# Optimization experiments

Hardware: AMD Instinct MI355X
Metric: run time of the kernel (lower is better)

The kernel has to match this reference:

```python
import jax, jax.numpy as jnp
import numpy as np

LIDAR_MAX_X = 32.0
LIDAR_MAX_Y = 32.0


def bilinear_grid_sample(value, grid):
    """torch.nn.functional.grid_sample, mode='bilinear', padding_mode='zeros',
    align_corners=False.
    value: (B, C, H, W); grid: (B, Q, P, 2) in [-1, 1] (x=width, y=height).
    Returns (B, C, Q, P)."""
    B, C, H, W = value.shape
    x = (grid[..., 0] + 1.0) * (W / 2) - 0.5  # (B,Q,P) unnormalized col
    y = (grid[..., 1] + 1.0) * (H / 2) - 0.5  # (B,Q,P) unnormalized row
    x0 = jnp.floor(x)
    y0 = jnp.floor(y)
    x1 = x0 + 1.0
    y1 = y0 + 1.0
    wx1 = x - x0
    wx0 = 1.0 - wx1
    wy1 = y - y0
    wy0 = 1.0 - wy1
    vflat = value.reshape(B, C, H * W)

    def gather(ix, iy):
        valid = (ix >= 0) & (ix <= W - 1) & (iy >= 0) & (iy <= H - 1)
        ixc = jnp.clip(ix, 0, W - 1).astype(jnp.int32)
        iyc = jnp.clip(iy, 0, H - 1).astype(jnp.int32)
        idx = iyc * W + ixc  # (B,Q,P)
        g = jax.vmap(lambda v, i: v[:, i])(vflat, idx)  # (B,C,Q,P)
        return g * valid[:, None, :, :].astype(value.dtype)

    out = (gather(x0, y0) * (wx0 * wy0)[:, None]
           + gather(x1, y0) * (wx1 * wy0)[:, None]
           + gather(x0, y1) * (wx0 * wy1)[:, None]
           + gather(x1, y1) * (wx1 * wy1)[:, None])
    return out


def setup_inputs() -> dict:
    key = jax.random.key(0)
    ks = jax.random.split(key, 10)
    bs, Q, P, D = 16, 1024, 8, 256
    Cin, H, W = 64, 128, 128
    queries = jax.random.normal(ks[0], (bs, Q, D), dtype=jnp.float32)
    # scale so trajectory points span the +/-32m BEV extent
    traj_points = jax.random.normal(ks[1], (bs, Q, P, 2), dtype=jnp.float32) * 20.0
    bev_feature = jax.random.normal(ks[2], (bs, Cin, H, W), dtype=jnp.float32)
    spatial_shape = jnp.array([H, W], dtype=jnp.int64)
    attn_w = jax.random.normal(ks[3], (P, D), dtype=jnp.float32) * 0.02
    attn_b = jnp.zeros((P,), dtype=jnp.float32)
    conv_w = jax.random.normal(ks[4], (256, Cin, 3, 3), dtype=jnp.float32) * 0.05
    conv_b = jnp.zeros((256,), dtype=jnp.float32)
    out_w = jax.random.normal(ks[5], (D, D), dtype=jnp.float32) * (1.0 / np.sqrt(D))
    out_b = jnp.zeros((D,), dtype=jnp.float32)
    return {"queries": queries, "traj_points": traj_points,
            "bev_feature": bev_feature, "spatial_shape": spatial_shape,
            "attn_w": attn_w, "attn_b": attn_b,
            "conv_w": conv_w, "conv_b": conv_b,
            "out_w": out_w, "out_b": out_b}


def reference(queries, traj_points, bev_feature, spatial_shape,
              attn_w, attn_b, conv_w, conv_b, out_w, out_b):
    # normalize trajectory to [-1,1] and swap (y,x) -> (x,y) grid order
    grid = jnp.stack([traj_points[..., 1] / LIDAR_MAX_X,
                      traj_points[..., 0] / LIDAR_MAX_Y], axis=-1)  # (bs,Q,P,2)
    # per-query attention over the P sampled points
    attn = jax.nn.softmax(
        jnp.einsum('bqd,pd->bqp', queries, attn_w) + attn_b, axis=-1)  # (bs,Q,P)
    # value projection: 3x3 conv + ReLU
    value = jax.lax.conv_general_dilated(
        bev_feature, conv_w, window_strides=(1, 1),
        padding=((1, 1), (1, 1)),
        dimension_numbers=('NCHW', 'OIHW', 'NCHW'))
    value = jax.nn.relu(value + conv_b[None, :, None, None])  # (bs,256,H,W)
    sampled = bilinear_grid_sample(value, grid)  # (bs,256,Q,P)
    out = jnp.einsum('bcqp,bqp->bqc', sampled, attn)  # weighted sum + permute
    out = jnp.einsum('bqc,dc->bqd', out, out_w) + out_b
    # dropout is identity in eval mode
    return out + queries
```

## Files before the change

### kernel.cpp

```cpp
#include <hip/hip_runtime.h>
#include <stdint.h>


typedef __attribute__((ext_vector_type(8))) short short8;
typedef __attribute__((ext_vector_type(4))) float f32x4;

__device__ __forceinline__ unsigned short f2bf(float f) {
  union { float f; unsigned int u; } v; v.f = f;
  unsigned int r = (v.u + 0x7FFFu + ((v.u >> 16) & 1u)) >> 16;
  return (unsigned short)r;
}
__device__ __forceinline__ float bf2f(unsigned short h) {
  union { unsigned int u; float f; } v; v.u = ((unsigned int)h) << 16;
  return v.f;
}

__device__ __forceinline__ void gload_lds16(const void* g, void* l) {
  __builtin_amdgcn_global_load_lds(
      (const __attribute__((address_space(1))) unsigned int*)g,
      (__attribute__((address_space(3))) unsigned int*)l, 16, 0, 0);
}

__global__ __launch_bounds__(256) void k1_transpose(const float* __restrict__ bev,
                                                    unsigned short* __restrict__ nhwc) {
  __shared__ __align__(16) float lds[64 * 32 * 4];
  const int b = blockIdx.x >> 7, y = blockIdx.x & 127;
  const int t = threadIdx.x;
  const float* src = bev + (size_t)(b * 64) * 16384 + y * 128;
#pragma unroll
  for (int k = 0; k < 8; ++k) {
    int chunk = k * 256 + t;
    int ic = chunk >> 5, xq = chunk & 31;
    float4 v = *(const float4*)(src + ic * 16384 + xq * 4);
    int slot = xq ^ (ic >> 3);
    *(float4*)&lds[(ic * 32 + slot) * 4] = v;
  }
  __syncthreads();
  unsigned short* dst = nhwc + (size_t)blockIdx.x * 8192;
#pragma unroll
  for (int k = 0; k < 4; ++k) {
    int co = k * 256 + t;
    int x = co >> 3, icg = co & 7;
    int slot = (x >> 2) ^ icg;
    int w = x & 3;
    uint4 u;
    unsigned int* up = (unsigned int*)&u;
#pragma unroll
    for (int jj = 0; jj < 4; ++jj) {
      float v0 = lds[((icg * 8 + 2 * jj) * 32 + slot) * 4 + w];
      float v1 = lds[((icg * 8 + 2 * jj + 1) * 32 + slot) * 4 + w];
      up[jj] = (unsigned int)f2bf(v0) | ((unsigned int)f2bf(v1) << 16);
    }
    *(uint4*)(dst + x * 64 + icg * 8) = u;
  }
}

__global__ __launch_bounds__(256) void k1b_pack(const float* __restrict__ conv_w,
                                                const float* __restrict__ out_w,
                                                unsigned short* __restrict__ wconv,
                                                unsigned short* __restrict__ wout,
                                                float* __restrict__ zp) {
  const int tid = blockIdx.x * 256 + threadIdx.x;
  for (int idx = tid; idx < 9 * 8 * 256 * 8; idx += 16384) {
    int j = idx & 7, oc = (idx >> 3) & 255, g = (idx >> 11) & 7, o = idx >> 14;
    wconv[idx] = f2bf(conv_w[(oc * 64 + g * 8 + j) * 9 + o]);
  }
  for (int idx = tid; idx < 32 * 256 * 8; idx += 16384) {
    int j = idx & 7, d = (idx >> 3) & 255, g = idx >> 11;
    wout[idx] = f2bf(out_w[d * 256 + g * 8 + j]);
  }
  if (tid < 64) zp[tid] = 0.0f;
}

#define K2_LOADA(s, A) do {                                                   \
    _Pragma("unroll")                                                         \
    for (int ocf_ = 0; ocf_ < 4; ++ocf_)                                      \
      A[ocf_] = gA[(4 * (s) + g) * 256 + ocb0 + ocf_ * 16 + l15];             \
  } while (0)

#define K2_READB(s, B) do {                                                   \
    const int o_ = (s) >> 1, ich_ = (s) & 1;                                  \
    const int dyr_ = o_ / 3, dx_ = o_ - dyr_ * 3 - 1;                         \
    _Pragma("unroll")                                                         \
    for (int pf_ = 0; pf_ < 4; ++pf_)                                         \
      B[pf_] = lin[(dyr_ * 8 + ich_ * 4 + g) * 130 + 1 + dx_ + xb +           \
                   pf_ * 16 + l15];                                           \
  } while (0)

#define K2_MF(A, B) do {                                                      \
    _Pragma("unroll")                                                         \
    for (int ocf_ = 0; ocf_ < 4; ++ocf_)                                      \
      _Pragma("unroll")                                                       \
      for (int pf_ = 0; pf_ < 4; ++pf_)                                       \
        acc[ocf_][pf_] = __builtin_amdgcn_mfma_f32_16x16x32_bf16(             \
            A[ocf_], B[pf_], acc[ocf_][pf_], 0, 0, 0);                        \
  } while (0)

__global__ __launch_bounds__(256, 3) void k2_conv(const unsigned short* __restrict__ nhwc,
                                                  const unsigned short* __restrict__ wconv,
                                                  const float* __restrict__ conv_b,
                                                  const float* __restrict__ zp,
                                                  unsigned short* __restrict__ value) {
  __shared__ __align__(16) char smem[50176];
  const short8* lin = (const short8*)smem;
  const short8* gA = (const short8*)wconv;
  const int bid = blockIdx.x;
  const int swz = (bid & 7) * 512 + (bid >> 3);
  const int b = swz >> 8, y = (swz >> 1) & 127, och = swz & 1;
  const int t = threadIdx.x, wid = t >> 6, lane = t & 63;
  const int wo = wid >> 1;
  const int xb = (wid & 1) * 64;
  const int g = lane >> 4, l15 = lane & 15;
  const int ocb0 = och * 128 + wo * 64;

  const unsigned short* bevb = nhwc + (size_t)b * (128 * 128 * 64);
  for (int i = wid; i < 49; i += 4) {
    const int chunk = i * 64 + lane;
    const void* src = (const void*)zp;
    if (chunk < 3120) {
      const int ridx = chunk / 1040;
      const int rem = chunk - ridx * 1040;
      const int icg = rem / 130;
      const int c = rem - icg * 130;
      const int yy = y - 1 + ridx, xx = c - 1;
      if (yy >= 0 && yy < 128 && xx >= 0 && xx < 128)
        src = (const void*)(bevb + ((yy * 128 + xx) * 64 + icg * 8));
    }
    gload_lds16(src, smem + i * 1024);
  }
  __syncthreads();

  const f32x4 z4 = {0.f, 0.f, 0.f, 0.f};
  f32x4 acc[4][4];
#pragma unroll
  for (int i = 0; i < 4; ++i)
#pragma unroll
    for (int j = 0; j < 4; ++j) acc[i][j] = z4;

  short8 A0[4], A1[4], B[4];
  K2_LOADA(0, A0);
  K2_LOADA(1, A1);

#pragma unroll
  for (int s = 0; s < 18; ++s) {
    K2_READB(s, B);
    __builtin_amdgcn_s_setprio(1);
    if (s & 1) {
      K2_MF(A1, B);
      __builtin_amdgcn_s_setprio(0);
      if (s + 2 < 18) K2_LOADA(s + 2, A1);
    } else {
      K2_MF(A0, B);
      __builtin_amdgcn_s_setprio(0);
      if (s + 2 < 18) K2_LOADA(s + 2, A0);
    }
  }

  unsigned short* vrow = value + (((size_t)(b * 128 + y) * 128 + xb + l15) * 256);
  float4 cb4[4];
#pragma unroll
  for (int ocf = 0; ocf < 4; ++ocf)
    cb4[ocf] = *(const float4*)(conv_b + ocb0 + ocf * 16 + g * 4);
#pragma unroll
  for (int pf = 0; pf < 4; ++pf) {
#pragma unroll
    for (int ocf = 0; ocf < 4; ++ocf) {
      const int ocb = ocb0 + ocf * 16 + g * 4;
      ushort4 ov;
      float v0 = acc[ocf][pf][0] + cb4[ocf].x; ov.x = f2bf(v0 > 0.f ? v0 : 0.f);
      float v1 = acc[ocf][pf][1] + cb4[ocf].y; ov.y = f2bf(v1 > 0.f ? v1 : 0.f);
      float v2 = acc[ocf][pf][2] + cb4[ocf].z; ov.z = f2bf(v2 > 0.f ? v2 : 0.f);
      float v3 = acc[ocf][pf][3] + cb4[ocf].w; ov.w = f2bf(v3 > 0.f ? v3 : 0.f);
      *(ushort4*)(vrow + (size_t)pf * 16 * 256 + ocb) = ov;
    }
  }
}

__global__ __launch_bounds__(256) void k3_sample(const float* __restrict__ queries,
                                                 const float* __restrict__ traj,
                                                 const float* __restrict__ attn_w,
                                                 const float* __restrict__ attn_b,
                                                 const unsigned short* __restrict__ value,
                                                 unsigned short* __restrict__ S) {
  const int wid = threadIdx.x >> 6, lane = threadIdx.x & 63;
  const int half = lane >> 5, hl = lane & 31;
  const int bid = blockIdx.x;
  const int sbid = (bid & 7) * 256 + (bid >> 3);
  const int qg = sbid * 8 + wid * 2 + half;
  const int b = qg >> 10;

  const float4 q0 = *(const float4*)(queries + (size_t)qg * 256 + hl * 8);
  const float4 q1 = *(const float4*)(queries + (size_t)qg * 256 + hl * 8 + 4);
  float a[8];
#pragma unroll
  for (int p = 0; p < 8; ++p) {
    const float4 w0 = *(const float4*)(attn_w + p * 256 + hl * 8);
    const float4 w1 = *(const float4*)(attn_w + p * 256 + hl * 8 + 4);
    float d = q0.x * w0.x + q0.y * w0.y + q0.z * w0.z + q0.w * w0.w
            + q1.x * w1.x + q1.y * w1.y + q1.z * w1.z + q1.w * w1.w;
#pragma unroll
    for (int off = 16; off >= 1; off >>= 1) d += __shfl_xor(d, off);
    a[p] = d + attn_b[p];
  }
  float mx = a[0];
#pragma unroll
  for (int p = 1; p < 8; ++p) mx = fmaxf(mx, a[p]);
  float ssum = 0.f;
#pragma unroll
  for (int p = 0; p < 8; ++p) { a[p] = __expf(a[p] - mx); ssum += a[p]; }
  const float inv = 1.f / ssum;

  float acc[8] = {0.f, 0.f, 0.f, 0.f, 0.f, 0.f, 0.f, 0.f};
  const unsigned short* vb = value + (size_t)b * (128 * 128 * 256);
#pragma unroll
  for (int p = 0; p < 8; ++p) {
    const float ty = traj[(qg * 8 + p) * 2 + 0];
    const float tx = traj[(qg * 8 + p) * 2 + 1];
    const float fx = (tx * 0.03125f + 1.f) * 64.f - 0.5f;
    const float fy = (ty * 0.03125f + 1.f) * 64.f - 0.5f;
    const float fx0 = floorf(fx), fy0 = floorf(fy);
    const int ix0 = (int)fx0, iy0 = (int)fy0;
    const float wx1 = fx - fx0, wx0 = 1.f - wx1;
    const float wy1 = fy - fy0, wy0 = 1.f - wy1;
    const float ap = a[p] * inv;
    const float cw[4] = {wx0 * wy0 * ap, wx1 * wy0 * ap, wx0 * wy1 * ap, wx1 * wy1 * ap};
#pragma unroll
    for (int cc = 0; cc < 4; ++cc) {
      const int cx = ix0 + (cc & 1), cy = iy0 + (cc >> 1);
      const bool valid = (cx >= 0) & (cx < 128) & (cy >= 0) & (cy < 128);
      const float w = valid ? cw[cc] : 0.f;
      const int cxc = min(max(cx, 0), 127), cyc = min(max(cy, 0), 127);
      const short8 v = *(const short8*)(vb + (cyc * 128 + cxc) * 256 + hl * 8);
#pragma unroll
      for (int j = 0; j < 8; ++j) acc[j] += w * bf2f((unsigned short)v[j]);
    }
  }
  short8 o;
#pragma unroll
  for (int j = 0; j < 8; ++j) o[j] = (short)f2bf(acc[j]);
  *(short8*)(S + (size_t)qg * 256 + hl * 8) = o;
}

__global__ __launch_bounds__(256) void k4_proj(const unsigned short* __restrict__ S,
                                               const unsigned short* __restrict__ wout,
                                               const float* __restrict__ out_b,
                                               const float* __restrict__ queries,
                                               float* __restrict__ out) {
  const short8* wp8 = (const short8*)wout;
  const short8* Sp = (const short8*)S;
  const int t = threadIdx.x, wid = t >> 6, lane = t & 63;
  const int q0 = blockIdx.x * 64;
  const int g = lane >> 4, l15 = lane & 15;
  const f32x4 z4 = {0.f, 0.f, 0.f, 0.f};
  f32x4 acc[4][4];
#pragma unroll
  for (int i = 0; i < 4; ++i)
#pragma unroll
    for (int j = 0; j < 4; ++j) acc[i][j] = z4;

#pragma unroll
  for (int ks = 0; ks < 8; ++ks) {
    short8 af[4];
#pragma unroll
    for (int df = 0; df < 4; ++df)
      af[df] = wp8[(ks * 4 + g) * 256 + wid * 64 + df * 16 + l15];
    short8 bf[4];
#pragma unroll
    for (int qf = 0; qf < 4; ++qf)
      bf[qf] = Sp[(size_t)(q0 + qf * 16 + l15) * 32 + ks * 4 + g];
#pragma unroll
    for (int df = 0; df < 4; ++df)
#pragma unroll
      for (int qf = 0; qf < 4; ++qf)
        acc[df][qf] = __builtin_amdgcn_mfma_f32_16x16x32_bf16(af[df], bf[qf], acc[df][qf], 0, 0, 0);
  }

#pragma unroll
  for (int df = 0; df < 4; ++df) {
    const int db = wid * 64 + df * 16 + g * 4;
    const float4 ob4 = *(const float4*)(out_b + db);
#pragma unroll
    for (int qf = 0; qf < 4; ++qf) {
      const int q = q0 + qf * 16 + l15;
      const float4 qv = *(const float4*)(queries + (size_t)q * 256 + db);
      float4 ov;
      ov.x = acc[df][qf][0] + ob4.x + qv.x;
      ov.y = acc[df][qf][1] + ob4.y + qv.y;
      ov.z = acc[df][qf][2] + ob4.z + qv.z;
      ov.w = acc[df][qf][3] + ob4.w + qv.w;
      *(float4*)(out + (size_t)q * 256 + db) = ov;
    }
  }
}

extern "C" void kernel_launch(void* const* d_in, const int* in_sizes, int n_in,
                              void* d_out, int out_size, void* d_ws, size_t ws_size,
                              hipStream_t stream) {
  const float* queries = (const float*)d_in[0];
  const float* traj    = (const float*)d_in[1];
  const float* bev     = (const float*)d_in[2];
  const float* attn_w  = (const float*)d_in[4];
  const float* attn_b  = (const float*)d_in[5];
  const float* conv_w  = (const float*)d_in[6];
  const float* conv_b  = (const float*)d_in[7];
  const float* out_w   = (const float*)d_in[8];
  const float* out_b   = (const float*)d_in[9];
  float* out = (float*)d_out;

  char* ws = (char*)d_ws;
  unsigned short* bev_nhwc = (unsigned short*)(ws);
  unsigned short* value    = (unsigned short*)(ws + 33554432);
  unsigned short* wconv    = (unsigned short*)(ws + 167772160);
  unsigned short* wout     = (unsigned short*)(ws + 168067072);
  unsigned short* Sbuf     = (unsigned short*)(ws + 168198144);
  float*          zp       = (float*)(ws + 176586752);

  k1_transpose<<<2048, 256, 0, stream>>>(bev, bev_nhwc);
  k1b_pack<<<64, 256, 0, stream>>>(conv_w, out_w, wconv, wout, zp);
  k2_conv<<<4096, 256, 0, stream>>>(bev_nhwc, wconv, conv_b, zp, value);
  k3_sample<<<2048, 256, 0, stream>>>(queries, traj, attn_w, attn_b, value, Sbuf);
  k4_proj<<<256, 256, 0, stream>>>(Sbuf, wout, out_b, queries, out);
}
```

Before: 161.4 us.

## Switch conv to 32x32x16 MFMA and compute full output row per block

The 3x3 conv kernel now uses 32x32x16 bf16 MFMA tiles instead of 16x16x32. Each block covers all 256 output channels for one image row, so the grid halves and the halo row staging into LDS happens once per row rather than twice. This reduces redundant LDS fills and raises per-instruction MFMA work. In exchange it uses more accumulator registers, lowering the occupancy hint from 3 to 2 blocks per CU, and it changes the output store pattern.

```diff
diff --git a/kernel.cpp b/kernel.cpp
--- a/kernel.cpp
+++ b/kernel.cpp
@@ -4,6 +4,7 @@
 
 typedef __attribute__((ext_vector_type(8))) short short8;
 typedef __attribute__((ext_vector_type(4))) float f32x4;
+typedef __attribute__((ext_vector_type(16))) float f32x16;
 
 __device__ __forceinline__ unsigned short f2bf(float f) {
   union { float f; unsigned int u; } v; v.f = f;
@@ -74,8 +75,11 @@
 
 #define K2_LOADA(s, A) do {                                                   \
     _Pragma("unroll")                                                         \
-    for (int ocf_ = 0; ocf_ < 4; ++ocf_)                                      \
-      A[ocf_] = gA[(4 * (s) + g) * 256 + ocb0 + ocf_ * 16 + l15];             \
+    for (int of_ = 0; of_ < 2; ++of_)                                         \
+      _Pragma("unroll")                                                       \
+      for (int kk_ = 0; kk_ < 2; ++kk_)                                       \
+        A[of_ * 2 + kk_] = gA[(4 * (s) + 2 * kk_ + h5) * 256 + wo * 64 +      \
+                              of_ * 32 + l31];                                \
   } while (0)
 
 #define K2_READB(s, B) do {                                                   \
@@ -83,20 +87,24 @@
     const int dyr_ = o_ / 3, dx_ = o_ - dyr_ * 3 - 1;                         \
     _Pragma("unroll")                                                         \
     for (int pf_ = 0; pf_ < 4; ++pf_)                                         \
-      B[pf_] = lin[(dyr_ * 8 + ich_ * 4 + g) * 130 + 1 + dx_ + xb +           \
-                   pf_ * 16 + l15];                                           \
+      _Pragma("unroll")                                                       \
+      for (int kk_ = 0; kk_ < 2; ++kk_)                                       \
+        B[pf_ * 2 + kk_] = lin[(dyr_ * 8 + ich_ * 4 + 2 * kk_ + h5) * 130 +   \
+                               1 + dx_ + pf_ * 32 + l31];                     \
   } while (0)
 
 #define K2_MF(A, B) do {                                                      \
     _Pragma("unroll")                                                         \
-    for (int ocf_ = 0; ocf_ < 4; ++ocf_)                                      \
+    for (int kk_ = 0; kk_ < 2; ++kk_)                                         \
       _Pragma("unroll")                                                       \
-      for (int pf_ = 0; pf_ < 4; ++pf_)                                       \
-        acc[ocf_][pf_] = __builtin_amdgcn_mfma_f32_16x16x32_bf16(             \
-            A[ocf_], B[pf_], acc[ocf_][pf_], 0, 0, 0);                        \
+      for (int of_ = 0; of_ < 2; ++of_)                                       \
+        _Pragma("unroll")                                                     \
+        for (int pf_ = 0; pf_ < 4; ++pf_)                                     \
+          acc[of_][pf_] = __builtin_amdgcn_mfma_f32_32x32x16_bf16(            \
+              A[of_ * 2 + kk_], B[pf_ * 2 + kk_], acc[of_][pf_], 0, 0, 0);    \
   } while (0)
 
-__global__ __launch_bounds__(256, 3) void k2_conv(const unsigned short* __restrict__ nhwc,
+__global__ __launch_bounds__(256, 2) void k2_conv(const unsigned short* __restrict__ nhwc,
                                                   const unsigned short* __restrict__ wconv,
                                                   const float* __restrict__ conv_b,
                                                   const float* __restrict__ zp,
@@ -105,13 +113,13 @@
   const short8* lin = (const short8*)smem;
   const short8* gA = (const short8*)wconv;
   const int bid = blockIdx.x;
-  const int swz = (bid & 7) * 512 + (bid >> 3);
-  const int b = swz >> 8, y = (swz >> 1) & 127, och = swz & 1;
+  const int swz = (bid & 7) * 256 + (bid >> 3);
+  const int b = swz >> 7, y = swz & 127;
   const int t = threadIdx.x, wid = t >> 6, lane = t & 63;
-  const int wo = wid >> 1;
-  const int xb = (wid & 1) * 64;
+  const int wo = wid;
+  const int h5 = lane >> 5, l31 = lane & 31;
   const int g = lane >> 4, l15 = lane & 15;
-  const int ocb0 = och * 128 + wo * 64;
+  (void)g; (void)l15;
 
   const unsigned short* bevb = nhwc + (size_t)b * (128 * 128 * 64);
   for (int i = wid; i < 49; i += 4) {
@@ -130,14 +138,15 @@
   }
   __syncthreads();
 
-  const f32x4 z4 = {0.f, 0.f, 0.f, 0.f};
-  f32x4 acc[4][4];
-#pragma unroll
-  for (int i = 0; i < 4; ++i)
-#pragma unroll
-    for (int j = 0; j < 4; ++j) acc[i][j] = z4;
-
-  short8 A0[4], A1[4], B[4];
+  f32x16 acc[2][4];
+#pragma unroll
+  for (int i = 0; i < 2; ++i)
+#pragma unroll
+    for (int j = 0; j < 4; ++j)
+#pragma unroll
+      for (int e = 0; e < 16; ++e) acc[i][j][e] = 0.f;
+
+  short8 A0[4], A1[4], B[8];
   K2_LOADA(0, A0);
   K2_LOADA(1, A1);
 
@@ -156,22 +165,24 @@
     }
   }
 
-  unsigned short* vrow = value + (((size_t)(b * 128 + y) * 128 + xb + l15) * 256);
-  float4 cb4[4];
-#pragma unroll
-  for (int ocf = 0; ocf < 4; ++ocf)
-    cb4[ocf] = *(const float4*)(conv_b + ocb0 + ocf * 16 + g * 4);
+  unsigned short* vbase = value + ((size_t)(b * 128 + y) * 128) * 256;
 #pragma unroll
   for (int pf = 0; pf < 4; ++pf) {
-#pragma unroll
-    for (int ocf = 0; ocf < 4; ++ocf) {
-      const int ocb = ocb0 + ocf * 16 + g * 4;
-      ushort4 ov;
-      float v0 = acc[ocf][pf][0] + cb4[ocf].x; ov.x = f2bf(v0 > 0.f ? v0 : 0.f);
-      float v1 = acc[ocf][pf][1] + cb4[ocf].y; ov.y = f2bf(v1 > 0.f ? v1 : 0.f);
-      float v2 = acc[ocf][pf][2] + cb4[ocf].z; ov.z = f2bf(v2 > 0.f ? v2 : 0.f);
-      float v3 = acc[ocf][pf][3] + cb4[ocf].w; ov.w = f2bf(v3 > 0.f ? v3 : 0.f);
-      *(ushort4*)(vrow + (size_t)pf * 16 * 256 + ocb) = ov;
+    const int pix = pf * 32 + l31;
+    unsigned short* vp = vbase + (size_t)pix * 256;
+#pragma unroll
+    for (int of = 0; of < 2; ++of) {
+#pragma unroll
+      for (int q = 0; q < 4; ++q) {
+        const int oc = wo * 64 + of * 32 + 4 * h5 + 8 * q;
+        const float4 cb = *(const float4*)(conv_b + oc);
+        ushort4 ov;
+        float v0 = acc[of][pf][q * 4 + 0] + cb.x; ov.x = f2bf(v0 > 0.f ? v0 : 0.f);
+        float v1 = acc[of][pf][q * 4 + 1] + cb.y; ov.y = f2bf(v1 > 0.f ? v1 : 0.f);
+        float v2 = acc[of][pf][q * 4 + 2] + cb.z; ov.z = f2bf(v2 > 0.f ? v2 : 0.f);
+        float v3 = acc[of][pf][q * 4 + 3] + cb.w; ov.w = f2bf(v3 > 0.f ? v3 : 0.f);
+        *(ushort4*)(vp + oc) = ov;
+      }
     }
   }
 }
@@ -317,7 +328,7 @@
 
   k1_transpose<<<2048, 256, 0, stream>>>(bev, bev_nhwc);
   k1b_pack<<<64, 256, 0, stream>>>(conv_w, out_w, wconv, wout, zp);
-  k2_conv<<<4096, 256, 0, stream>>>(bev_nhwc, wconv, conv_b, zp, value);
+  k2_conv<<<2048, 256, 0, stream>>>(bev_nhwc, wconv, conv_b, zp, value);
   k3_sample<<<2048, 256, 0, stream>>>(queries, traj, attn_w, attn_b, value, Sbuf);
   k4_proj<<<256, 256, 0, stream>>>(Sbuf, wout, out_b, queries, out);
 }
```

Result: faster. 157.2 us (-2.6%).
